# Kernel optimization log

Measured on AMD Instinct MI355X. Metric: run time of the kernel, lower is better.

Reference implementation:

```python
import jax, jax.numpy as jnp
import numpy as np

HEAD = 8
AGENT = 64  # agent_q_num = agent_kv_num = 8**2
DIM = 512


def _heads(t, head=HEAD):
    b, n, c = t.shape
    return t.reshape(b, n, head, c // head).transpose(0, 2, 1, 3)  # (b,h,n,d)


def _attn(q, k, v, pe, scale):
    # post-softmax additive bias (the non-standard part that breaks SDPA fusion)
    s = jax.nn.softmax(jnp.einsum('bhnd,bhmd->bhnm', q, k) * scale, axis=-1) + pe
    o = jnp.einsum('bhnm,bhmd->bhnd', s, v)
    b, h, n, d = o.shape
    return o.transpose(0, 2, 1, 3).reshape(b, n, h * d)


def _mlp(x, w1, b1, w2, b2):
    return jax.nn.silu(x @ w1 + b1) @ w2 + b2


def setup_inputs() -> dict:
    key = jax.random.key(0)
    ks = jax.random.split(key, 32)
    d = DIM
    inp = {
        'x': jax.random.normal(ks[0], (8, 64, 64, d), jnp.float32),
        'learnable_q': jax.random.normal(ks[1], (1, AGENT, d), jnp.float32) * 0.02,
        'learnable_kv': jax.random.normal(ks[2], (1, AGENT, d), jnp.float32) * 0.02,
        'pe1': jax.random.normal(ks[3], (1, HEAD, 1, AGENT), jnp.float32) * 0.02,
        'pe2': jax.random.normal(ks[4], (1, HEAD, AGENT, 1), jnp.float32) * 0.02,
        'w_q': jax.random.normal(ks[5], (d, d), jnp.float32) * (d ** -0.5),
        'b_q': jax.random.normal(ks[6], (d,), jnp.float32) * 0.02,
        'w_kvx': jax.random.normal(ks[7], (d, 2 * d), jnp.float32) * (d ** -0.5),
        'b_kvx': jax.random.normal(ks[8], (2 * d,), jnp.float32) * 0.02,
        'w_kvy': jax.random.normal(ks[9], (d, 2 * d), jnp.float32) * (d ** -0.5),
        'b_kvy': jax.random.normal(ks[10], (2 * d,), jnp.float32) * 0.02,
        'w_q2': jax.random.normal(ks[11], (d, d), jnp.float32) * (d ** -0.5),
        'b_q2': jax.random.normal(ks[12], (d,), jnp.float32) * 0.02,
        'f1w1': jax.random.normal(ks[13], (d, d), jnp.float32) * (d ** -0.5),
        'f1b1': jax.random.normal(ks[14], (d,), jnp.float32) * 0.02,
        'f1w2': jax.random.normal(ks[15], (d, d), jnp.float32) * (d ** -0.5),
        'f1b2': jax.random.normal(ks[16], (d,), jnp.float32) * 0.02,
        'f2w1': jax.random.normal(ks[17], (d, d), jnp.float32) * (d ** -0.5),
        'f2b1': jax.random.normal(ks[18], (d,), jnp.float32) * 0.02,
        'f2w2': jax.random.normal(ks[19], (d, d), jnp.float32) * (d ** -0.5),
        'f2b2': jax.random.normal(ks[20], (d,), jnp.float32) * 0.02,
    }
    return inp


def reference(x, learnable_q, learnable_kv, pe1, pe2, w_q, b_q, w_kvx, b_kvx,
              w_kvy, b_kvy, w_q2, b_q2, f1w1, f1b1, f1w2, f1b2,
              f2w1, f2b1, f2w2, f2b2):
    b, h, w, c = x.shape
    d = c // HEAD
    scale = d ** -0.5
    xf = x.reshape(b, h * w, c)

    # stage 1: image tokens attend to learnable proxy kv tokens
    q = _heads(xf @ w_q2 + b_q2)                                   # (b,H,hw,d)
    kv = jnp.broadcast_to(learnable_kv, (b, AGENT, c)) @ w_kvy + b_kvy
    k, v = jnp.split(kv, 2, axis=-1)
    out = _attn(q, _heads(k), _heads(v), pe1, scale)               # (b,hw,c)
    out = _mlp(out, f1w1, f1b1, f1w2, f1b2) + xf
    mskip = out

    # stage 2: learnable proxy queries attend to image tokens
    q2 = _heads(jnp.broadcast_to(learnable_q, (b, AGENT, c)) @ w_q + b_q)
    kv = out @ w_kvx + b_kvx
    k, v = jnp.split(kv, 2, axis=-1)
    fin = _attn(q2, _heads(k), _heads(v), pe2, scale)              # (b,AGENT,c)
    fin = _mlp(fin, f2w1, f2b1, f2w2, f2b2)

    # nearest-neighbor upsample 8x8 agent grid back to (h,w)
    s = int(AGENT ** 0.5)
    fin = fin.reshape(b, s, s, c)
    fin = jnp.repeat(jnp.repeat(fin, h // s, axis=1), w // s, axis=2)
    return fin + mskip.reshape(b, h, w, c) + x
```

## Files before the change

### kernel.cpp

```cpp
#include <hip/hip_runtime.h>
#include <stdint.h>

typedef unsigned short ub16;
typedef __attribute__((ext_vector_type(8))) short short8;
typedef __attribute__((ext_vector_type(4))) float f32x4;
typedef __attribute__((ext_vector_type(4))) unsigned short us4v;

__device__ __forceinline__ float bf2f(ub16 u) {
  union { unsigned int i; float f; } v; v.i = ((unsigned int)u) << 16; return v.f;
}
__device__ __forceinline__ ub16 f2bf(float f) {
  union { float f; unsigned int i; } v; v.f = f;
  return (ub16)((v.i + 0x7FFFu + ((v.i >> 16) & 1u)) >> 16);
}
__device__ __forceinline__ f32x4 zero4() { f32x4 v = {0.f, 0.f, 0.f, 0.f}; return v; }
__device__ __forceinline__ f32x4 mfma16(short8 a, short8 b, f32x4 c) {
  return __builtin_amdgcn_mfma_f32_16x16x32_bf16(a, b, c, 0, 0, 0);
}
__device__ __forceinline__ float rmax16(float x) {
  x = fmaxf(x, __shfl_xor(x, 1)); x = fmaxf(x, __shfl_xor(x, 2));
  x = fmaxf(x, __shfl_xor(x, 4)); x = fmaxf(x, __shfl_xor(x, 8)); return x;
}
__device__ __forceinline__ float rsum16(float x) {
  x += __shfl_xor(x, 1); x += __shfl_xor(x, 2);
  x += __shfl_xor(x, 4); x += __shfl_xor(x, 8); return x;
}

__device__ __forceinline__ void gload16(const ub16* g, ub16* l) {
  __builtin_amdgcn_global_load_lds(
      (const __attribute__((address_space(1))) void*)g,
      (__attribute__((address_space(3))) void*)l, 16, 0, 0);
}

__device__ __forceinline__ void stage_tile(const ub16* __restrict__ src, ub16* ldsbase,
                                           int wid, int lane) {
  const int rr = lane >> 3;
  const int slog = (lane & 7) ^ rr;
#pragma unroll
  for (int c = 0; c < 4; ++c) {
    int chunk = wid * 4 + c;
    int row = chunk * 8 + rr;
    gload16(src + (size_t)row * 512 + slog * 8,
            (ub16*)((char*)ldsbase + chunk * 1024));
  }
}

__device__ __forceinline__ void gemm_compute(const ub16* Ab, const ub16* Bb, int wm, int wn,
                                             int l15, int lg, f32x4 acc[4][4]) {
#pragma unroll
  for (int kf = 0; kf < 2; ++kf) {
    short8 af[4], bfr[4];
#pragma unroll
    for (int mf = 0; mf < 4; ++mf) {
      int row = wm * 64 + mf * 16 + l15;
      af[mf] = *(const short8*)((const char*)Ab + row * 128 +
                                ((kf * 64 + lg * 16) ^ ((row & 7) << 4)));
    }
#pragma unroll
    for (int nf = 0; nf < 4; ++nf) {
      int row = wn * 64 + nf * 16 + l15;
      bfr[nf] = *(const short8*)((const char*)Bb + row * 128 +
                                 ((kf * 64 + lg * 16) ^ ((row & 7) << 4)));
    }
#pragma unroll
    for (int mf = 0; mf < 4; ++mf)
#pragma unroll
      for (int nf = 0; nf < 4; ++nf)
        acc[mf][nf] = mfma16(af[mf], bfr[nf], acc[mf][nf]);
  }
}

__device__ __forceinline__ void gemm_k512(const ub16* Ap, const ub16* Bp, ub16* lds,
                                          int wid, int lane, int wm, int wn, int l15, int lg,
                                          f32x4 acc[4][4]) {
  ub16* A0 = lds;
  ub16* B0 = lds + 8192;
#pragma unroll
  for (int kb = 0; kb < 8; ++kb) {
    stage_tile(Ap + kb * 64, A0, wid, lane);
    stage_tile(Bp + kb * 64, B0, wid, lane);
    asm volatile("s_waitcnt vmcnt(0)" ::: "memory");
    __syncthreads();
    gemm_compute(A0, B0, wm, wn, l15, lg, acc);
    __syncthreads();
  }
}

__device__ __forceinline__ void xcd_remap(int nx, int& m0, int& n0) {
  int bid = blockIdx.x, nwg = gridDim.x;
  int cpx = nwg >> 3;
  int wgid = (bid & 7) * cpx + (bid >> 3);
  n0 = (wgid % nx) * 128;
  m0 = (wgid / nx) * 128;
}

__global__ void k_cvt(const float* __restrict__ x, ub16* __restrict__ xb) {
  int i = blockIdx.x * 256 + threadIdx.x;
  f32x4 v = *(const f32x4*)&x[(size_t)i * 4];
  us4v o;
#pragma unroll
  for (int e = 0; e < 4; ++e) o[e] = f2bf(v[e]);
  *(us4v*)&xb[(size_t)i * 4] = o;
}

__global__ void k_prep_wt(const float* s0, const float* s1, const float* s2,
                          const float* s3, const float* s4,
                          ub16* d0, ub16* d1, ub16* d2, ub16* d3, ub16* d4) {
  const float* src; ub16* dst; int N;
  switch (blockIdx.z) {
    case 0: src = s0; dst = d0; N = 512; break;
    case 1: src = s1; dst = d1; N = 512; break;
    case 2: src = s2; dst = d2; N = 512; break;
    case 3: src = s3; dst = d3; N = 512; break;
    default: src = s4; dst = d4; N = 1024; break;
  }
  int n0 = blockIdx.x * 64, k0 = blockIdx.y * 64;
  if (n0 >= N) return;
  __shared__ float tile[64][65];
#pragma unroll
  for (int i = 0; i < 16; ++i) {
    int idx = i * 256 + threadIdx.x, r = idx >> 6, c = idx & 63;
    tile[r][c] = src[(size_t)(k0 + r) * N + n0 + c];
  }
  __syncthreads();
#pragma unroll
  for (int i = 0; i < 16; ++i) {
    int idx = i * 256 + threadIdx.x, r = idx >> 6, c = idx & 63;
    dst[(size_t)(n0 + r) * 512 + k0 + c] = f2bf(tile[c][r]);
  }
}

__global__ void k_prep_small(const float* __restrict__ lkv, const float* __restrict__ w_kvy,
                             const float* __restrict__ b_kvy, const float* __restrict__ lq,
                             const float* __restrict__ w_q, const float* __restrict__ b_q,
                             const float* __restrict__ pe1,
                             ub16* __restrict__ k1, ub16* __restrict__ v1T,
                             float* __restrict__ bias1, ub16* __restrict__ q2p) {
  int j = blockIdx.x, t = threadIdx.x;
  __shared__ float wcol[512];
  __shared__ float red[64];
  const float* W; const float* src; float bias; int NC, jj;
  if (j < 1024) { W = w_kvy; NC = 1024; src = lkv; jj = j;        bias = b_kvy[j]; }
  else          { W = w_q;   NC = 512;  src = lq;  jj = j - 1024; bias = b_q[jj]; }
#pragma unroll
  for (int e = 0; e < 8; ++e) wcol[t * 8 + e] = W[(size_t)(t * 8 + e) * NC + jj];
  __syncthreads();
  float acc = bias;
  for (int k = 0; k < 512; ++k) acc += src[(size_t)t * 512 + k] * wcol[k];
  if (j < 512) {
    int h = j >> 6, d = j & 63;
    k1[(size_t)(h * 64 + t) * 64 + d] = f2bf(acc * 0.125f);
  } else if (j < 1024) {
    int h = (j - 512) >> 6, d = (j - 512) & 63;
    v1T[(size_t)(h * 64 + d) * 64 + t] = f2bf(acc);
    red[t] = pe1[h * 64 + t] * acc;
    __syncthreads();
    for (int s = 32; s > 0; s >>= 1) { if (t < s) red[t] += red[t + s]; __syncthreads(); }
    if (t == 0) bias1[h * 64 + d] = red[0];
  } else {
    int h = jj >> 6, d = jj & 63;
    q2p[(size_t)(h * 64 + t) * 64 + d] = f2bf(acc * 0.125f);
  }
}

__global__ __launch_bounds__(256) void k_prep_wqk(
    const float* __restrict__ w_q2, const float* __restrict__ b_q2,
    const ub16* __restrict__ k1, ub16* __restrict__ WqkT,
    float* __restrict__ biass) {
  int ha = blockIdx.x, h = ha >> 6, t = threadIdx.x;
  __shared__ float kr[64];
  if (t < 64) kr[t] = bf2f(k1[(size_t)ha * 64 + t]);
  __syncthreads();
#pragma unroll
  for (int i = 0; i < 2; ++i) {
    int kin = t + i * 256;
    const float* wrow = &w_q2[(size_t)kin * 512 + h * 64];
    float acc = 0.f;
#pragma unroll
    for (int d4 = 0; d4 < 16; ++d4) {
      f32x4 wv = *(const f32x4*)&wrow[d4 * 4];
      acc += wv[0] * kr[d4 * 4] + wv[1] * kr[d4 * 4 + 1] +
             wv[2] * kr[d4 * 4 + 2] + wv[3] * kr[d4 * 4 + 3];
    }
    WqkT[(size_t)ha * 512 + kin] = f2bf(acc);
  }
  if (t == 0) {
    float acc = 0.f;
    for (int d = 0; d < 64; ++d) acc += b_q2[h * 64 + d] * kr[d];
    biass[ha] = acc;
  }
}

__global__ __launch_bounds__(256) void k_s1a(
    const ub16* __restrict__ xb, const ub16* __restrict__ WqkT,
    const float* __restrict__ biass, const ub16* __restrict__ v1T,
    const float* __restrict__ bias1, ub16* __restrict__ o1) {
  __shared__ ub16 lds[16384];
  const int tid = threadIdx.x, lane = tid & 63, wid = tid >> 6;
  const int wm = wid >> 1, wn = wid & 1;
  const int l15 = lane & 15, lg = lane >> 4;
  int m0, n0;
  xcd_remap(4, m0, n0);

  f32x4 acc[4][4];
#pragma unroll
  for (int a = 0; a < 4; ++a)
#pragma unroll
    for (int b = 0; b < 4; ++b) acc[a][b] = zero4();

  gemm_k512(xb + (size_t)m0 * 512, WqkT + (size_t)n0 * 512, lds,
            wid, lane, wm, wn, l15, lg, acc);

  __syncthreads();
  const int h = (n0 >> 6) + wn;
  char* Pl = (char*)lds + wid * 8192;
  float bsv[4];
#pragma unroll
  for (int nf = 0; nf < 4; ++nf) bsv[nf] = biass[h * 64 + nf * 16 + l15];
  float dinv[4][4];
#pragma unroll
  for (int mf = 0; mf < 4; ++mf) {
#pragma unroll
    for (int r = 0; r < 4; ++r) {
      float s0 = acc[mf][0][r] + bsv[0], s1 = acc[mf][1][r] + bsv[1];
      float s2 = acc[mf][2][r] + bsv[2], s3 = acc[mf][3][r] + bsv[3];
      float mx = rmax16(fmaxf(fmaxf(s0, s1), fmaxf(s2, s3)));
      float p0 = __expf(s0 - mx), p1 = __expf(s1 - mx);
      float p2 = __expf(s2 - mx), p3 = __expf(s3 - mx);
      float sm = rsum16(p0 + p1 + p2 + p3);
      dinv[mf][r] = 1.0f / sm;
      int tr = mf * 16 + lg * 4 + r;
      char* rb = Pl + tr * 128;
      int sw = (tr & 7) << 4;
      *(ub16*)(rb + (((0 * 16 + l15) * 2) ^ sw)) = f2bf(p0);
      *(ub16*)(rb + (((1 * 16 + l15) * 2) ^ sw)) = f2bf(p1);
      *(ub16*)(rb + (((2 * 16 + l15) * 2) ^ sw)) = f2bf(p2);
      *(ub16*)(rb + (((3 * 16 + l15) * 2) ^ sw)) = f2bf(p3);
    }
  }
  short8 pa[4][2], vb[4][2];
#pragma unroll
  for (int mf = 0; mf < 4; ++mf) {
    int row = mf * 16 + l15;
#pragma unroll
    for (int kf = 0; kf < 2; ++kf)
      pa[mf][kf] = *(const short8*)(Pl + row * 128 + ((kf * 64 + lg * 16) ^ ((row & 7) << 4)));
  }
#pragma unroll
  for (int nf = 0; nf < 4; ++nf)
#pragma unroll
    for (int kf = 0; kf < 2; ++kf)
      vb[nf][kf] = *(const short8*)&v1T[(size_t)(h * 64 + nf * 16 + l15) * 64 + kf * 32 + lg * 8];
  f32x4 oacc[4][4];
#pragma unroll
  for (int a = 0; a < 4; ++a)
#pragma unroll
    for (int b = 0; b < 4; ++b) oacc[a][b] = zero4();
#pragma unroll
  for (int kf = 0; kf < 2; ++kf)
#pragma unroll
    for (int mf = 0; mf < 4; ++mf)
#pragma unroll
      for (int nf = 0; nf < 4; ++nf)
        oacc[mf][nf] = mfma16(pa[mf][kf], vb[nf][kf], oacc[mf][nf]);
  float b1v[4];
#pragma unroll
  for (int nf = 0; nf < 4; ++nf) b1v[nf] = bias1[h * 64 + nf * 16 + l15];
#pragma unroll
  for (int mf = 0; mf < 4; ++mf)
#pragma unroll
    for (int nf = 0; nf < 4; ++nf)
#pragma unroll
      for (int r = 0; r < 4; ++r) {
        float val = oacc[mf][nf][r] * dinv[mf][r] + b1v[nf];
        o1[(size_t)(m0 + wm * 64 + mf * 16 + lg * 4 + r) * 512 + h * 64 + nf * 16 + l15] = f2bf(val);
      }
}

__global__ __launch_bounds__(256) void k_mlp1a(
    const ub16* __restrict__ o1, const ub16* __restrict__ W1T,
    const float* __restrict__ b1, ub16* __restrict__ h1) {
  __shared__ ub16 lds[16384];
  const int tid = threadIdx.x, lane = tid & 63, wid = tid >> 6;
  const int wm = wid >> 1, wn = wid & 1;
  const int l15 = lane & 15, lg = lane >> 4;
  int m0, n0;
  xcd_remap(4, m0, n0);
  f32x4 acc[4][4];
#pragma unroll
  for (int a = 0; a < 4; ++a)
#pragma unroll
    for (int b = 0; b < 4; ++b) acc[a][b] = zero4();
  gemm_k512(o1 + (size_t)m0 * 512, W1T + (size_t)n0 * 512, lds,
            wid, lane, wm, wn, l15, lg, acc);
#pragma unroll
  for (int nf = 0; nf < 4; ++nf) {
    int n = n0 + wn * 64 + nf * 16 + l15;
    float bb = b1[n];
#pragma unroll
    for (int mf = 0; mf < 4; ++mf)
#pragma unroll
      for (int r = 0; r < 4; ++r) {
        float v = acc[mf][nf][r] + bb;
        v = v / (1.0f + __expf(-v));
        int m = m0 + wm * 64 + mf * 16 + lg * 4 + r;
        h1[(size_t)m * 512 + n] = f2bf(v);
      }
  }
}

__global__ __launch_bounds__(256) void k_mlp1b(
    const ub16* __restrict__ h1, const ub16* __restrict__ W2T,
    const float* __restrict__ b2, ub16* __restrict__ xb_mskip) {
  __shared__ ub16 lds[16384];
  const int tid = threadIdx.x, lane = tid & 63, wid = tid >> 6;
  const int wm = wid >> 1, wn = wid & 1;
  const int l15 = lane & 15, lg = lane >> 4;
  int m0, n0;
  xcd_remap(4, m0, n0);
  f32x4 acc[4][4];
#pragma unroll
  for (int a = 0; a < 4; ++a)
#pragma unroll
    for (int b = 0; b < 4; ++b) acc[a][b] = zero4();
  gemm_k512(h1 + (size_t)m0 * 512, W2T + (size_t)n0 * 512, lds,
            wid, lane, wm, wn, l15, lg, acc);
#pragma unroll
  for (int nf = 0; nf < 4; ++nf) {
    int n = n0 + wn * 64 + nf * 16 + l15;
    float bb = b2[n];
#pragma unroll
    for (int mf = 0; mf < 4; ++mf)
#pragma unroll
      for (int r = 0; r < 4; ++r) {
        int m = m0 + wm * 64 + mf * 16 + lg * 4 + r;
        size_t idx = (size_t)m * 512 + n;
        float val = acc[mf][nf][r] + bb + bf2f(xb_mskip[idx]);
        xb_mskip[idx] = f2bf(val);
      }
  }
}

__global__ __launch_bounds__(256) void k_mlp2b(
    const ub16* __restrict__ h2, const ub16* __restrict__ W2T,
    const float* __restrict__ b2, float* __restrict__ fin) {
  __shared__ ub16 lds[16384];
  const int tid = threadIdx.x, lane = tid & 63, wid = tid >> 6;
  const int wm = wid >> 1, wn = wid & 1;
  const int l15 = lane & 15, lg = lane >> 4;
  int m0, n0;
  xcd_remap(4, m0, n0);
  f32x4 acc[4][4];
#pragma unroll
  for (int a = 0; a < 4; ++a)
#pragma unroll
    for (int b = 0; b < 4; ++b) acc[a][b] = zero4();
  gemm_k512(h2 + (size_t)m0 * 512, W2T + (size_t)n0 * 512, lds,
            wid, lane, wm, wn, l15, lg, acc);
#pragma unroll
  for (int nf = 0; nf < 4; ++nf) {
    int n = n0 + wn * 64 + nf * 16 + l15;
    float bb = b2[n];
#pragma unroll
    for (int mf = 0; mf < 4; ++mf)
#pragma unroll
      for (int r = 0; r < 4; ++r) {
        int m = m0 + wm * 64 + mf * 16 + lg * 4 + r;
        fin[(size_t)m * 512 + n] = acc[mf][nf][r] + bb;
      }
  }
}

__global__ __launch_bounds__(256) void k_g4(
    const ub16* __restrict__ mskip_bf, const ub16* __restrict__ WT,
    const float* __restrict__ bias, ub16* __restrict__ Kb, ub16* __restrict__ VTb) {
  __shared__ ub16 lds[16384];
  const int tid = threadIdx.x, lane = tid & 63, wid = tid >> 6;
  const int wm = wid >> 1, wn = wid & 1;
  const int l15 = lane & 15, lg = lane >> 4;
  int m0, n0;
  xcd_remap(8, m0, n0);
  f32x4 acc[4][4];
#pragma unroll
  for (int a = 0; a < 4; ++a)
#pragma unroll
    for (int b = 0; b < 4; ++b) acc[a][b] = zero4();
  gemm_k512(mskip_bf + (size_t)m0 * 512, WT + (size_t)n0 * 512, lds,
            wid, lane, wm, wn, l15, lg, acc);
  const int ncb = n0 + wn * 64;
  if (n0 < 512) {
    const int hh = ncb >> 6;
#pragma unroll
    for (int mf = 0; mf < 4; ++mf)
#pragma unroll
      for (int r = 0; r < 4; ++r) {
        int m = m0 + wm * 64 + mf * 16 + lg * 4 + r;
        int b = m >> 12, t = m & 4095;
#pragma unroll
        for (int nf = 0; nf < 4; ++nf) {
          int d = nf * 16 + l15;
          Kb[((size_t)(b * 8 + hh) * 4096 + t) * 64 + d] = f2bf(acc[mf][nf][r] + bias[ncb + d]);
        }
      }
  } else {
    const int hv = (ncb >> 6) - 8;
#pragma unroll
    for (int mf = 0; mf < 4; ++mf) {
      int m4 = m0 + wm * 64 + mf * 16 + lg * 4;
      int b = m4 >> 12, t = m4 & 4095;
#pragma unroll
      for (int nf = 0; nf < 4; ++nf) {
        int d = nf * 16 + l15;
        float bb = bias[ncb + d];
        us4v pk;
#pragma unroll
        for (int r = 0; r < 4; ++r) pk[r] = f2bf(acc[mf][nf][r] + bb);
        *(us4v*)&VTb[((size_t)(b * 8 + hv) * 64 + d) * 4096 + t] = pk;
      }
    }
  }
}

__global__ __launch_bounds__(256) void k_attn2(
    const ub16* __restrict__ q2p, const ub16* __restrict__ Kb, const ub16* __restrict__ VTb,
    float* __restrict__ m_part, float* __restrict__ l_part,
    float* __restrict__ cs_part, float* __restrict__ o_part) {
  const int tid = threadIdx.x, lane = tid & 63, wid = tid >> 6;
  const int l15 = lane & 15, lg = lane >> 4;
  const int b = blockIdx.z, h = blockIdx.y;
  const int split = blockIdx.x * 4 + wid;
  __shared__ ub16 plds[4 * 64 * 40];
  ub16* pl = plds + wid * 64 * 40;
  short8 qa[4][2];
#pragma unroll
  for (int mf = 0; mf < 4; ++mf)
#pragma unroll
    for (int kf = 0; kf < 2; ++kf)
      qa[mf][kf] = *(const short8*)&q2p[(size_t)(h * 64 + mf * 16 + l15) * 64 + kf * 32 + lg * 8];
  float mr[4][4], lr[4][4], cs[4] = {0.f, 0.f, 0.f, 0.f};
  f32x4 oa[4][4];
#pragma unroll
  for (int a = 0; a < 4; ++a)
#pragma unroll
    for (int r = 0; r < 4; ++r) { mr[a][r] = -1e30f; lr[a][r] = 0.f; }
#pragma unroll
  for (int a = 0; a < 4; ++a)
#pragma unroll
    for (int n = 0; n < 4; ++n) oa[a][n] = zero4();
  const size_t kbase = (size_t)(b * 8 + h) * 4096 * 64;
  const size_t vbase = (size_t)(b * 8 + h) * 64 * 4096;
  for (int c = 0; c < 8; ++c) {
    int tb = split * 256 + c * 32;
    short8 kbf[2][2];
#pragma unroll
    for (int nf = 0; nf < 2; ++nf)
#pragma unroll
      for (int kf = 0; kf < 2; ++kf)
        kbf[nf][kf] = *(const short8*)&Kb[kbase + (size_t)(tb + nf * 16 + l15) * 64 + kf * 32 + lg * 8];
    f32x4 sc[4][2];
#pragma unroll
    for (int a = 0; a < 4; ++a)
#pragma unroll
      for (int n = 0; n < 2; ++n) sc[a][n] = zero4();
#pragma unroll
    for (int kf = 0; kf < 2; ++kf)
#pragma unroll
      for (int mf = 0; mf < 4; ++mf)
#pragma unroll
        for (int nf = 0; nf < 2; ++nf)
          sc[mf][nf] = mfma16(qa[mf][kf], kbf[nf][kf], sc[mf][nf]);
    float al[4][4];
#pragma unroll
    for (int mf = 0; mf < 4; ++mf)
#pragma unroll
      for (int r = 0; r < 4; ++r) {
        float cm = rmax16(fmaxf(sc[mf][0][r], sc[mf][1][r]));
        float nm = fmaxf(mr[mf][r], cm);
        float a_ = __expf(mr[mf][r] - nm);
        float p0 = __expf(sc[mf][0][r] - nm), p1 = __expf(sc[mf][1][r] - nm);
        float rs = rsum16(p0 + p1);
        lr[mf][r] = lr[mf][r] * a_ + rs;
        mr[mf][r] = nm;
        al[mf][r] = a_;
        int ar = mf * 16 + lg * 4 + r;
        char* rb = (char*)pl + ar * 80;
        *(ub16*)(rb + (0 * 16 + l15) * 2) = f2bf(p0);
        *(ub16*)(rb + (1 * 16 + l15) * 2) = f2bf(p1);
      }
#pragma unroll
    for (int mf = 0; mf < 4; ++mf)
#pragma unroll
      for (int nf = 0; nf < 4; ++nf)
#pragma unroll
        for (int r = 0; r < 4; ++r) oa[mf][nf][r] *= al[mf][r];
    short8 pa[4], vb[4];
#pragma unroll
    for (int mf = 0; mf < 4; ++mf)
      pa[mf] = *(const short8*)((char*)pl + (mf * 16 + l15) * 80 + lg * 16);
#pragma unroll
    for (int nf = 0; nf < 4; ++nf) {
      vb[nf] = *(const short8*)&VTb[vbase + (size_t)(nf * 16 + l15) * 4096 + tb + lg * 8];
#pragma unroll
      for (int e = 0; e < 8; ++e) cs[nf] += bf2f((ub16)vb[nf][e]);
    }
#pragma unroll
    for (int mf = 0; mf < 4; ++mf)
#pragma unroll
      for (int nf = 0; nf < 4; ++nf)
        oa[mf][nf] = mfma16(pa[mf], vb[nf], oa[mf][nf]);
  }
#pragma unroll
  for (int nf = 0; nf < 4; ++nf) {
    cs[nf] += __shfl_xor(cs[nf], 16);
    cs[nf] += __shfl_xor(cs[nf], 32);
  }
  const int pidx = (b * 8 + h) * 16 + split;
  if (lg == 0) {
#pragma unroll
    for (int nf = 0; nf < 4; ++nf) cs_part[(size_t)pidx * 64 + nf * 16 + l15] = cs[nf];
  }
  if (l15 == 0) {
#pragma unroll
    for (int mf = 0; mf < 4; ++mf)
#pragma unroll
      for (int r = 0; r < 4; ++r) {
        int a = mf * 16 + lg * 4 + r;
        m_part[(size_t)pidx * 64 + a] = mr[mf][r];
        l_part[(size_t)pidx * 64 + a] = lr[mf][r];
      }
  }
#pragma unroll
  for (int mf = 0; mf < 4; ++mf)
#pragma unroll
    for (int nf = 0; nf < 4; ++nf)
#pragma unroll
      for (int r = 0; r < 4; ++r) {
        int a = mf * 16 + lg * 4 + r, d = nf * 16 + l15;
        o_part[(size_t)pidx * 4096 + a * 64 + d] = oa[mf][nf][r];
      }
}

__global__ __launch_bounds__(256) void k_combine(
    const float* __restrict__ m_part, const float* __restrict__ l_part,
    const float* __restrict__ cs_part, const float* __restrict__ o_part,
    const float* __restrict__ pe2, ub16* __restrict__ fin0) {
  int bh = blockIdx.x, b = bh >> 3, h = bh & 7;
  int t = threadIdx.x;
  __shared__ float wsp[16][64];
  __shared__ float linv[64];
  __shared__ float cst[64];
  int base = bh * 16;
  if (t < 64) {
    int a = t;
    float M = -1e30f;
    for (int s = 0; s < 16; ++s) M = fmaxf(M, m_part[(size_t)(base + s) * 64 + a]);
    float L = 0.f;
    for (int s = 0; s < 16; ++s) {
      float w = __expf(m_part[(size_t)(base + s) * 64 + a] - M);
      wsp[s][a] = w;
      L += l_part[(size_t)(base + s) * 64 + a] * w;
    }
    linv[a] = 1.0f / L;
  } else if (t < 128) {
    int d = t - 64;
    float c = 0.f;
    for (int s = 0; s < 16; ++s) c += cs_part[(size_t)(base + s) * 64 + d];
    cst[d] = c;
  }
  __syncthreads();
#pragma unroll
  for (int e0 = 0; e0 < 4096; e0 += 256) {
    int e = e0 + t, a = e >> 6, d = e & 63;
    float acc = 0.f;
#pragma unroll
    for (int s = 0; s < 16; ++s) acc += o_part[(size_t)(base + s) * 4096 + e] * wsp[s][a];
    float val = acc * linv[a] + pe2[h * 64 + a] * cst[d];
    fin0[(size_t)(b * 64 + a) * 512 + h * 64 + d] = f2bf(val);
  }
}

__global__ void k_final(const float* __restrict__ x, const float* __restrict__ fin,
                        const ub16* __restrict__ mskip_bf, float* __restrict__ out) {
  int i = blockIdx.x * 256 + threadIdx.x;
  int e = i * 4;
  int c = e & 511, j = (e >> 9) & 63, ii = (e >> 15) & 63, b = e >> 21;
  f32x4 xv = *(const f32x4*)&x[(size_t)e];
  us4v mv = *(const us4v*)&mskip_bf[(size_t)e];
  f32x4 fv = *(const f32x4*)&fin[(size_t)((b * 64 + (ii >> 3) * 8 + (j >> 3)) << 9) + c];
  f32x4 r;
#pragma unroll
  for (int q = 0; q < 4; ++q) r[q] = xv[q] + fv[q] + bf2f(mv[q]);
  *(f32x4*)&out[(size_t)e] = r;
}

extern "C" void kernel_launch(void* const* d_in, const int* in_sizes, int n_in,
                              void* d_out, int out_size, void* d_ws, size_t ws_size,
                              hipStream_t stream) {
  const float* x     = (const float*)d_in[0];
  const float* lq    = (const float*)d_in[1];
  const float* lkv   = (const float*)d_in[2];
  const float* pe1   = (const float*)d_in[3];
  const float* pe2   = (const float*)d_in[4];
  const float* w_q   = (const float*)d_in[5];
  const float* b_q   = (const float*)d_in[6];
  const float* w_kvx = (const float*)d_in[7];
  const float* b_kvx = (const float*)d_in[8];
  const float* w_kvy = (const float*)d_in[9];
  const float* b_kvy = (const float*)d_in[10];
  const float* w_q2  = (const float*)d_in[11];
  const float* b_q2  = (const float*)d_in[12];
  const float* f1w1  = (const float*)d_in[13];
  const float* f1b1  = (const float*)d_in[14];
  const float* f1w2  = (const float*)d_in[15];
  const float* f1b2  = (const float*)d_in[16];
  const float* f2w1  = (const float*)d_in[17];
  const float* f2b1  = (const float*)d_in[18];
  const float* f2w2  = (const float*)d_in[19];
  const float* f2b2  = (const float*)d_in[20];
  float* out = (float*)d_out;

  char* ws = (char*)d_ws;
  size_t off = 0;
  auto alloc = [&](size_t bytes) {
    char* p = ws + off;
    off += (bytes + 255) & ~(size_t)255;
    return p;
  };
  ub16* xb    = (ub16*)alloc((size_t)32768 * 512 * 2);
  ub16* o1    = (ub16*)alloc((size_t)32768 * 512 * 2);
  ub16* VTb   = (ub16*)alloc((size_t)64 * 64 * 4096 * 2);
  ub16* WqkT  = (ub16*)alloc((size_t)512 * 512 * 2);
  ub16* w1T   = (ub16*)alloc((size_t)512 * 512 * 2);
  ub16* w2T   = (ub16*)alloc((size_t)512 * 512 * 2);
  ub16* g1T   = (ub16*)alloc((size_t)512 * 512 * 2);
  ub16* g2T   = (ub16*)alloc((size_t)512 * 512 * 2);
  ub16* kvxT  = (ub16*)alloc((size_t)1024 * 512 * 2);
  ub16* k1    = (ub16*)alloc((size_t)8 * 64 * 64 * 2);
  ub16* v1T   = (ub16*)alloc((size_t)8 * 64 * 64 * 2);
  ub16* q2p   = (ub16*)alloc((size_t)8 * 64 * 64 * 2);
  float* bias1 = (float*)alloc(512 * 4);
  float* biass = (float*)alloc(512 * 4);
  float* m_part = (float*)alloc((size_t)1024 * 64 * 4);
  float* l_part = (float*)alloc((size_t)1024 * 64 * 4);
  float* cs_part = (float*)alloc((size_t)1024 * 64 * 4);
  float* o_part = (float*)alloc((size_t)1024 * 4096 * 4);
  ub16* fin0 = (ub16*)alloc((size_t)512 * 512 * 2);
  float* fin = (float*)alloc((size_t)512 * 512 * 4);
  ub16* h2 = (ub16*)alloc((size_t)512 * 512 * 2);
  ub16* Kbuf = o1;
  ub16* h1buf = VTb;
  ub16* mskip_bf = xb;
  (void)in_sizes; (void)n_in; (void)out_size; (void)ws_size;

  const int n4 = (8 * 64 * 64 * 512) / 4;

  k_cvt<<<n4 / 256, 256, 0, stream>>>(x, xb);
  k_prep_wt<<<dim3(16, 8, 5), 256, 0, stream>>>(f1w1, f1w2, f2w1, f2w2, w_kvx,
                                                w1T, w2T, g1T, g2T, kvxT);
  k_prep_small<<<1536, 64, 0, stream>>>(lkv, w_kvy, b_kvy, lq, w_q, b_q, pe1,
                                        k1, v1T, bias1, q2p);
  k_prep_wqk<<<512, 256, 0, stream>>>(w_q2, b_q2, k1, WqkT, biass);
  k_s1a<<<1024, 256, 0, stream>>>(xb, WqkT, biass, v1T, bias1, o1);
  k_mlp1a<<<1024, 256, 0, stream>>>(o1, w1T, f1b1, h1buf);
  k_mlp1b<<<1024, 256, 0, stream>>>(h1buf, w2T, f1b2, mskip_bf);
  k_g4<<<2048, 256, 0, stream>>>(mskip_bf, kvxT, b_kvx, Kbuf, VTb);
  k_attn2<<<dim3(4, 8, 8), 256, 0, stream>>>(q2p, Kbuf, VTb, m_part, l_part, cs_part, o_part);
  k_combine<<<64, 256, 0, stream>>>(m_part, l_part, cs_part, o_part, pe2, fin0);
  k_mlp1a<<<16, 256, 0, stream>>>(fin0, g1T, f2b1, h2);
  k_mlp2b<<<16, 256, 0, stream>>>(h2, g2T, f2b2, fin);
  k_final<<<n4 / 256, 256, 0, stream>>>(x, fin, mskip_bf, out);
}
```

Before: 332.2 us.

## Use 256x128 tiles with 8 waves and swapped MFMA operands for vectorized epilogues

The MLP and KV projection GEMMs move from 128x128 tiles with 4 waves to 256x128 tiles with 8 waves, so each staged B tile serves twice as many rows and B-side global traffic drops. MFMA operands are swapped so each lane holds four consecutive columns, letting bias loads and output stores use 4-wide vector accesses instead of scalar strided stores. The cost is larger LDS use per block, fewer blocks in flight, and the tiny stage-2 MLP launches now use only 8 blocks.

Result: slower. 341.7 us (+2.8%).

```diff
diff --git a/kernel.cpp b/kernel.cpp
--- a/kernel.cpp
+++ b/kernel.cpp
@@ -39,6 +39,20 @@
 #pragma unroll
   for (int c = 0; c < 4; ++c) {
     int chunk = wid * 4 + c;
+    int row = chunk * 8 + rr;
+    gload16(src + (size_t)row * 512 + slog * 8,
+            (ub16*)((char*)ldsbase + chunk * 1024));
+  }
+}
+
+template<int CNT>
+__device__ __forceinline__ void stage_tile512(const ub16* __restrict__ src, ub16* ldsbase,
+                                              int wid, int lane) {
+  const int rr = lane >> 3;
+  const int slog = (lane & 7) ^ rr;
+#pragma unroll
+  for (int c = 0; c < CNT; ++c) {
+    int chunk = c * 8 + wid;
     int row = chunk * 8 + rr;
     gload16(src + (size_t)row * 512 + slog * 8,
             (ub16*)((char*)ldsbase + chunk * 1024));
@@ -86,12 +100,63 @@
   }
 }
 
+template<bool SWAP>
+__device__ __forceinline__ void gemm_compute_w8(const ub16* Ab, const ub16* Bb, int wm, int wn,
+                                                int l15, int lg, f32x4 acc[4][4]) {
+#pragma unroll
+  for (int kf = 0; kf < 2; ++kf) {
+    short8 af[4], bfr[4];
+#pragma unroll
+    for (int mf = 0; mf < 4; ++mf) {
+      int row = wm * 64 + mf * 16 + l15;
+      af[mf] = *(const short8*)((const char*)Ab + row * 128 +
+                                ((kf * 64 + lg * 16) ^ ((row & 7) << 4)));
+    }
+#pragma unroll
+    for (int nf = 0; nf < 4; ++nf) {
+      int row = wn * 64 + nf * 16 + l15;
+      bfr[nf] = *(const short8*)((const char*)Bb + row * 128 +
+                                 ((kf * 64 + lg * 16) ^ ((row & 7) << 4)));
+    }
+#pragma unroll
+    for (int mf = 0; mf < 4; ++mf)
+#pragma unroll
+      for (int nf = 0; nf < 4; ++nf)
+        acc[mf][nf] = SWAP ? mfma16(bfr[nf], af[mf], acc[mf][nf])
+                           : mfma16(af[mf], bfr[nf], acc[mf][nf]);
+  }
+}
+
+template<bool SWAP>
+__device__ __forceinline__ void gemm_k512_w8(const ub16* Ap, const ub16* Bp, ub16* lds,
+                                             int wid, int lane, int wm, int wn, int l15, int lg,
+                                             f32x4 acc[4][4]) {
+  ub16* A0 = lds;
+  ub16* B0 = lds + 16384;
+#pragma unroll
+  for (int kb = 0; kb < 8; ++kb) {
+    stage_tile512<4>(Ap + kb * 64, A0, wid, lane);
+    stage_tile512<2>(Bp + kb * 64, B0, wid, lane);
+    asm volatile("s_waitcnt vmcnt(0)" ::: "memory");
+    __syncthreads();
+    gemm_compute_w8<SWAP>(A0, B0, wm, wn, l15, lg, acc);
+    __syncthreads();
+  }
+}
+
 __device__ __forceinline__ void xcd_remap(int nx, int& m0, int& n0) {
   int bid = blockIdx.x, nwg = gridDim.x;
   int cpx = nwg >> 3;
   int wgid = (bid & 7) * cpx + (bid >> 3);
   n0 = (wgid % nx) * 128;
   m0 = (wgid / nx) * 128;
+}
+__device__ __forceinline__ void xcd_remap256(int nx, int& m0, int& n0) {
+  int bid = blockIdx.x, nwg = gridDim.x;
+  int cpx = nwg >> 3;
+  int wgid = (bid & 7) * cpx + (bid >> 3);
+  n0 = (wgid % nx) * 128;
+  m0 = (wgid / nx) * 256;
 }
 
 __global__ void k_cvt(const float* __restrict__ x, ub16* __restrict__ xb) {
@@ -277,132 +342,142 @@
       }
 }
 
-__global__ __launch_bounds__(256) void k_mlp1a(
-    const ub16* __restrict__ o1, const ub16* __restrict__ W1T,
+__global__ __launch_bounds__(512) void k_mlp1a(
+    const ub16* __restrict__ in, const ub16* __restrict__ W1T,
     const float* __restrict__ b1, ub16* __restrict__ h1) {
-  __shared__ ub16 lds[16384];
+  __shared__ ub16 lds[24576];
   const int tid = threadIdx.x, lane = tid & 63, wid = tid >> 6;
   const int wm = wid >> 1, wn = wid & 1;
   const int l15 = lane & 15, lg = lane >> 4;
   int m0, n0;
-  xcd_remap(4, m0, n0);
+  xcd_remap256(4, m0, n0);
   f32x4 acc[4][4];
 #pragma unroll
   for (int a = 0; a < 4; ++a)
 #pragma unroll
     for (int b = 0; b < 4; ++b) acc[a][b] = zero4();
-  gemm_k512(o1 + (size_t)m0 * 512, W1T + (size_t)n0 * 512, lds,
-            wid, lane, wm, wn, l15, lg, acc);
-#pragma unroll
-  for (int nf = 0; nf < 4; ++nf) {
-    int n = n0 + wn * 64 + nf * 16 + l15;
-    float bb = b1[n];
-#pragma unroll
-    for (int mf = 0; mf < 4; ++mf)
+  gemm_k512_w8<true>(in + (size_t)m0 * 512, W1T + (size_t)n0 * 512, lds,
+                     wid, lane, wm, wn, l15, lg, acc);
+#pragma unroll
+  for (int mf = 0; mf < 4; ++mf) {
+    int m = m0 + wm * 64 + mf * 16 + l15;
+#pragma unroll
+    for (int nf = 0; nf < 4; ++nf) {
+      int nb = n0 + wn * 64 + nf * 16 + lg * 4;
+      f32x4 bb = *(const f32x4*)&b1[nb];
+      us4v pk;
 #pragma unroll
       for (int r = 0; r < 4; ++r) {
-        float v = acc[mf][nf][r] + bb;
+        float v = acc[mf][nf][r] + bb[r];
         v = v / (1.0f + __expf(-v));
-        int m = m0 + wm * 64 + mf * 16 + lg * 4 + r;
-        h1[(size_t)m * 512 + n] = f2bf(v);
+        pk[r] = f2bf(v);
       }
-  }
-}
-
-__global__ __launch_bounds__(256) void k_mlp1b(
+      *(us4v*)&h1[(size_t)m * 512 + nb] = pk;
+    }
+  }
+}
+
+__global__ __launch_bounds__(512) void k_mlp1b(
     const ub16* __restrict__ h1, const ub16* __restrict__ W2T,
     const float* __restrict__ b2, ub16* __restrict__ xb_mskip) {
-  __shared__ ub16 lds[16384];
+  __shared__ ub16 lds[24576];
   const int tid = threadIdx.x, lane = tid & 63, wid = tid >> 6;
   const int wm = wid >> 1, wn = wid & 1;
   const int l15 = lane & 15, lg = lane >> 4;
   int m0, n0;
-  xcd_remap(4, m0, n0);
+  xcd_remap256(4, m0, n0);
   f32x4 acc[4][4];
 #pragma unroll
   for (int a = 0; a < 4; ++a)
 #pragma unroll
     for (int b = 0; b < 4; ++b) acc[a][b] = zero4();
-  gemm_k512(h1 + (size_t)m0 * 512, W2T + (size_t)n0 * 512, lds,
-            wid, lane, wm, wn, l15, lg, acc);
-#pragma unroll
-  for (int nf = 0; nf < 4; ++nf) {
-    int n = n0 + wn * 64 + nf * 16 + l15;
-    float bb = b2[n];
-#pragma unroll
-    for (int mf = 0; mf < 4; ++mf)
-#pragma unroll
-      for (int r = 0; r < 4; ++r) {
-        int m = m0 + wm * 64 + mf * 16 + lg * 4 + r;
-        size_t idx = (size_t)m * 512 + n;
-        float val = acc[mf][nf][r] + bb + bf2f(xb_mskip[idx]);
-        xb_mskip[idx] = f2bf(val);
-      }
-  }
-}
-
-__global__ __launch_bounds__(256) void k_mlp2b(
+  gemm_k512_w8<true>(h1 + (size_t)m0 * 512, W2T + (size_t)n0 * 512, lds,
+                     wid, lane, wm, wn, l15, lg, acc);
+#pragma unroll
+  for (int mf = 0; mf < 4; ++mf) {
+    int m = m0 + wm * 64 + mf * 16 + l15;
+#pragma unroll
+    for (int nf = 0; nf < 4; ++nf) {
+      int nb = n0 + wn * 64 + nf * 16 + lg * 4;
+      f32x4 bb = *(const f32x4*)&b2[nb];
+      size_t idx = (size_t)m * 512 + nb;
+      us4v mv = *(const us4v*)&xb_mskip[idx];
+      us4v pk;
+#pragma unroll
+      for (int r = 0; r < 4; ++r)
+        pk[r] = f2bf(acc[mf][nf][r] + bb[r] + bf2f(mv[r]));
+      *(us4v*)&xb_mskip[idx] = pk;
+    }
+  }
+}
+
+__global__ __launch_bounds__(512) void k_mlp2b(
     const ub16* __restrict__ h2, const ub16* __restrict__ W2T,
     const float* __restrict__ b2, float* __restrict__ fin) {
-  __shared__ ub16 lds[16384];
+  __shared__ ub16 lds[24576];
   const int tid = threadIdx.x, lane = tid & 63, wid = tid >> 6;
   const int wm = wid >> 1, wn = wid & 1;
   const int l15 = lane & 15, lg = lane >> 4;
   int m0, n0;
-  xcd_remap(4, m0, n0);
+  xcd_remap256(4, m0, n0);
   f32x4 acc[4][4];
 #pragma unroll
   for (int a = 0; a < 4; ++a)
 #pragma unroll
     for (int b = 0; b < 4; ++b) acc[a][b] = zero4();
-  gemm_k512(h2 + (size_t)m0 * 512, W2T + (size_t)n0 * 512, lds,
-            wid, lane, wm, wn, l15, lg, acc);
-#pragma unroll
-  for (int nf = 0; nf < 4; ++nf) {
-    int n = n0 + wn * 64 + nf * 16 + l15;
-    float bb = b2[n];
-#pragma unroll
-    for (int mf = 0; mf < 4; ++mf)
-#pragma unroll
-      for (int r = 0; r < 4; ++r) {
-        int m = m0 + wm * 64 + mf * 16 + lg * 4 + r;
-        fin[(size_t)m * 512 + n] = acc[mf][nf][r] + bb;
-      }
-  }
-}
-
-__global__ __launch_bounds__(256) void k_g4(
+  gemm_k512_w8<true>(h2 + (size_t)m0 * 512, W2T + (size_t)n0 * 512, lds,
+                     wid, lane, wm, wn, l15, lg, acc);
+#pragma unroll
+  for (int mf = 0; mf < 4; ++mf) {
+    int m = m0 + wm * 64 + mf * 16 + l15;
+#pragma unroll
+    for (int nf = 0; nf < 4; ++nf) {
+      int nb = n0 + wn * 64 + nf * 16 + lg * 4;
+      f32x4 bb = *(const f32x4*)&b2[nb];
+      f32x4 ov;
+#pragma unroll
+      for (int r = 0; r < 4; ++r) ov[r] = acc[mf][nf][r] + bb[r];
+      *(f32x4*)&fin[(size_t)m * 512 + nb] = ov;
+    }
+  }
+}
+
+__global__ __launch_bounds__(512) void k_g4(
     const ub16* __restrict__ mskip_bf, const ub16* __restrict__ WT,
     const float* __restrict__ bias, ub16* __restrict__ Kb, ub16* __restrict__ VTb) {
-  __shared__ ub16 lds[16384];
+  __shared__ ub16 lds[24576];
   const int tid = threadIdx.x, lane = tid & 63, wid = tid >> 6;
   const int wm = wid >> 1, wn = wid & 1;
   const int l15 = lane & 15, lg = lane >> 4;
   int m0, n0;
-  xcd_remap(8, m0, n0);
+  xcd_remap256(8, m0, n0);
   f32x4 acc[4][4];
 #pragma unroll
   for (int a = 0; a < 4; ++a)
 #pragma unroll
     for (int b = 0; b < 4; ++b) acc[a][b] = zero4();
-  gemm_k512(mskip_bf + (size_t)m0 * 512, WT + (size_t)n0 * 512, lds,
-            wid, lane, wm, wn, l15, lg, acc);
   const int ncb = n0 + wn * 64;
   if (n0 < 512) {
+    gemm_k512_w8<true>(mskip_bf + (size_t)m0 * 512, WT + (size_t)n0 * 512, lds,
+                       wid, lane, wm, wn, l15, lg, acc);
     const int hh = ncb >> 6;
 #pragma unroll
-    for (int mf = 0; mf < 4; ++mf)
-#pragma unroll
-      for (int r = 0; r < 4; ++r) {
-        int m = m0 + wm * 64 + mf * 16 + lg * 4 + r;
-        int b = m >> 12, t = m & 4095;
-#pragma unroll
-        for (int nf = 0; nf < 4; ++nf) {
-          int d = nf * 16 + l15;
-          Kb[((size_t)(b * 8 + hh) * 4096 + t) * 64 + d] = f2bf(acc[mf][nf][r] + bias[ncb + d]);
-        }
+    for (int mf = 0; mf < 4; ++mf) {
+      int m = m0 + wm * 64 + mf * 16 + l15;
+      int b = m >> 12, t = m & 4095;
+#pragma unroll
+      for (int nf = 0; nf < 4; ++nf) {
+        int d0 = nf * 16 + lg * 4;
+        f32x4 bb = *(const f32x4*)&bias[ncb + d0];
+        us4v pk;
+#pragma unroll
+        for (int r = 0; r < 4; ++r) pk[r] = f2bf(acc[mf][nf][r] + bb[r]);
+        *(us4v*)&Kb[((size_t)(b * 8 + hh) * 4096 + t) * 64 + d0] = pk;
       }
+    }
   } else {
+    gemm_k512_w8<false>(mskip_bf + (size_t)m0 * 512, WT + (size_t)n0 * 512, lds,
+                        wid, lane, wm, wn, l15, lg, acc);
     const int hv = (ncb >> 6) - 8;
 #pragma unroll
     for (int mf = 0; mf < 4; ++mf) {
@@ -661,12 +736,12 @@
                                         k1, v1T, bias1, q2p);
   k_prep_wqk<<<512, 256, 0, stream>>>(w_q2, b_q2, k1, WqkT, biass);
   k_s1a<<<1024, 256, 0, stream>>>(xb, WqkT, biass, v1T, bias1, o1);
-  k_mlp1a<<<1024, 256, 0, stream>>>(o1, w1T, f1b1, h1buf);
-  k_mlp1b<<<1024, 256, 0, stream>>>(h1buf, w2T, f1b2, mskip_bf);
-  k_g4<<<2048, 256, 0, stream>>>(mskip_bf, kvxT, b_kvx, Kbuf, VTb);
+  k_mlp1a<<<512, 512, 0, stream>>>(o1, w1T, f1b1, h1buf);
+  k_mlp1b<<<512, 512, 0, stream>>>(h1buf, w2T, f1b2, mskip_bf);
+  k_g4<<<1024, 512, 0, stream>>>(mskip_bf, kvxT, b_kvx, Kbuf, VTb);
   k_attn2<<<dim3(4, 8, 8), 256, 0, stream>>>(q2p, Kbuf, VTb, m_part, l_part, cs_part, o_part);
   k_combine<<<64, 256, 0, stream>>>(m_part, l_part, cs_part, o_part, pe2, fin0);
-  k_mlp1a<<<16, 256, 0, stream>>>(fin0, g1T, f2b1, h2);
-  k_mlp2b<<<16, 256, 0, stream>>>(h2, g2T, f2b2, fin);
+  k_mlp1a<<<8, 512, 0, stream>>>(fin0, g1T, f2b1, h2);
+  k_mlp2b<<<8, 512, 0, stream>>>(h2, g2T, f2b2, fin);
   k_final<<<n4 / 256, 256, 0, stream>>>(x, fin, mskip_bf, out);
 }
```

## Fuse fp32-to-bf16 conversion of x into stage-1 GEMM and vectorize epilogues

Applied to the files above, without the earlier changes.

Removes the standalone k_cvt pass by having k_s1a load fp32 x directly and convert to bf16 while staging into LDS. The mlp1b residual now reads fp32 x instead of the bf16 copy. GEMM epilogues swap MFMA operand order so each lane holds four consecutive columns, which allows vectorized bias loads and 8/16-byte stores. This trades the async global_load_lds path for synchronous register loads of the A tile in k_s1a, which may reduce load/compute overlap.

Result: no change. 327.3 us (-1.5%).

```diff
diff --git a/kernel.cpp b/kernel.cpp
--- a/kernel.cpp
+++ b/kernel.cpp
@@ -45,6 +45,25 @@
   }
 }
 
+__device__ __forceinline__ void stage_a_f32(const float* __restrict__ src, ub16* ldsbase,
+                                            int wid, int lane) {
+  const int rr = lane >> 3;
+  const int slot = lane & 7;
+#pragma unroll
+  for (int c = 0; c < 4; ++c) {
+    int chunk = wid * 4 + c;
+    int row = chunk * 8 + rr;
+    const float* g = src + (size_t)row * 512 + slot * 8;
+    f32x4 v0 = *(const f32x4*)g;
+    f32x4 v1 = *(const f32x4*)(g + 4);
+    short8 sv;
+#pragma unroll
+    for (int e = 0; e < 4; ++e) { sv[e] = (short)f2bf(v0[e]); sv[4 + e] = (short)f2bf(v1[e]); }
+    *(short8*)((char*)ldsbase + row * 128 + ((slot * 16) ^ ((row & 7) << 4))) = sv;
+  }
+}
+
+template<bool SWAP>
 __device__ __forceinline__ void gemm_compute(const ub16* Ab, const ub16* Bb, int wm, int wn,
                                              int l15, int lg, f32x4 acc[4][4]) {
 #pragma unroll
@@ -66,10 +85,12 @@
     for (int mf = 0; mf < 4; ++mf)
 #pragma unroll
       for (int nf = 0; nf < 4; ++nf)
-        acc[mf][nf] = mfma16(af[mf], bfr[nf], acc[mf][nf]);
-  }
-}
-
+        acc[mf][nf] = SWAP ? mfma16(bfr[nf], af[mf], acc[mf][nf])
+                           : mfma16(af[mf], bfr[nf], acc[mf][nf]);
+  }
+}
+
+template<bool SWAP>
 __device__ __forceinline__ void gemm_k512(const ub16* Ap, const ub16* Bp, ub16* lds,
                                           int wid, int lane, int wm, int wn, int l15, int lg,
                                           f32x4 acc[4][4]) {
@@ -81,7 +102,23 @@
     stage_tile(Bp + kb * 64, B0, wid, lane);
     asm volatile("s_waitcnt vmcnt(0)" ::: "memory");
     __syncthreads();
-    gemm_compute(A0, B0, wm, wn, l15, lg, acc);
+    gemm_compute<SWAP>(A0, B0, wm, wn, l15, lg, acc);
+    __syncthreads();
+  }
+}
+
+__device__ __forceinline__ void gemm_k512_af32(const float* Ap, const ub16* Bp, ub16* lds,
+                                               int wid, int lane, int wm, int wn, int l15, int lg,
+                                               f32x4 acc[4][4]) {
+  ub16* A0 = lds;
+  ub16* B0 = lds + 8192;
+#pragma unroll
+  for (int kb = 0; kb < 8; ++kb) {
+    stage_tile(Bp + kb * 64, B0, wid, lane);
+    stage_a_f32(Ap + kb * 64, A0, wid, lane);
+    asm volatile("s_waitcnt vmcnt(0)" ::: "memory");
+    __syncthreads();
+    gemm_compute<false>(A0, B0, wm, wn, l15, lg, acc);
     __syncthreads();
   }
 }
@@ -92,15 +129,6 @@
   int wgid = (bid & 7) * cpx + (bid >> 3);
   n0 = (wgid % nx) * 128;
   m0 = (wgid / nx) * 128;
-}
-
-__global__ void k_cvt(const float* __restrict__ x, ub16* __restrict__ xb) {
-  int i = blockIdx.x * 256 + threadIdx.x;
-  f32x4 v = *(const f32x4*)&x[(size_t)i * 4];
-  us4v o;
-#pragma unroll
-  for (int e = 0; e < 4; ++e) o[e] = f2bf(v[e]);
-  *(us4v*)&xb[(size_t)i * 4] = o;
 }
 
 __global__ void k_prep_wt(const float* s0, const float* s1, const float* s2,
@@ -192,7 +220,7 @@
 }
 
 __global__ __launch_bounds__(256) void k_s1a(
-    const ub16* __restrict__ xb, const ub16* __restrict__ WqkT,
+    const float* __restrict__ x, const ub16* __restrict__ WqkT,
     const float* __restrict__ biass, const ub16* __restrict__ v1T,
     const float* __restrict__ bias1, ub16* __restrict__ o1) {
   __shared__ ub16 lds[16384];
@@ -208,8 +236,8 @@
 #pragma unroll
     for (int b = 0; b < 4; ++b) acc[a][b] = zero4();
 
-  gemm_k512(xb + (size_t)m0 * 512, WqkT + (size_t)n0 * 512, lds,
-            wid, lane, wm, wn, l15, lg, acc);
+  gemm_k512_af32(x + (size_t)m0 * 512, WqkT + (size_t)n0 * 512, lds,
+                 wid, lane, wm, wn, l15, lg, acc);
 
   __syncthreads();
   const int h = (n0 >> 6) + wn;
@@ -278,7 +306,7 @@
 }
 
 __global__ __launch_bounds__(256) void k_mlp1a(
-    const ub16* __restrict__ o1, const ub16* __restrict__ W1T,
+    const ub16* __restrict__ in, const ub16* __restrict__ W1T,
     const float* __restrict__ b1, ub16* __restrict__ h1) {
   __shared__ ub16 lds[16384];
   const int tid = threadIdx.x, lane = tid & 63, wid = tid >> 6;
@@ -291,27 +319,31 @@
   for (int a = 0; a < 4; ++a)
 #pragma unroll
     for (int b = 0; b < 4; ++b) acc[a][b] = zero4();
-  gemm_k512(o1 + (size_t)m0 * 512, W1T + (size_t)n0 * 512, lds,
-            wid, lane, wm, wn, l15, lg, acc);
-#pragma unroll
-  for (int nf = 0; nf < 4; ++nf) {
-    int n = n0 + wn * 64 + nf * 16 + l15;
-    float bb = b1[n];
-#pragma unroll
-    for (int mf = 0; mf < 4; ++mf)
+  gemm_k512<true>(in + (size_t)m0 * 512, W1T + (size_t)n0 * 512, lds,
+                  wid, lane, wm, wn, l15, lg, acc);
+#pragma unroll
+  for (int mf = 0; mf < 4; ++mf) {
+    int m = m0 + wm * 64 + mf * 16 + l15;
+#pragma unroll
+    for (int nf = 0; nf < 4; ++nf) {
+      int nb = n0 + wn * 64 + nf * 16 + lg * 4;
+      f32x4 bb = *(const f32x4*)&b1[nb];
+      us4v pk;
 #pragma unroll
       for (int r = 0; r < 4; ++r) {
-        float v = acc[mf][nf][r] + bb;
+        float v = acc[mf][nf][r] + bb[r];
         v = v / (1.0f + __expf(-v));
-        int m = m0 + wm * 64 + mf * 16 + lg * 4 + r;
-        h1[(size_t)m * 512 + n] = f2bf(v);
+        pk[r] = f2bf(v);
       }
+      *(us4v*)&h1[(size_t)m * 512 + nb] = pk;
+    }
   }
 }
 
 __global__ __launch_bounds__(256) void k_mlp1b(
     const ub16* __restrict__ h1, const ub16* __restrict__ W2T,
-    const float* __restrict__ b2, ub16* __restrict__ xb_mskip) {
+    const float* __restrict__ b2, const float* __restrict__ x,
+    ub16* __restrict__ mskip) {
   __shared__ ub16 lds[16384];
   const int tid = threadIdx.x, lane = tid & 63, wid = tid >> 6;
   const int wm = wid >> 1, wn = wid & 1;
@@ -323,21 +355,22 @@
   for (int a = 0; a < 4; ++a)
 #pragma unroll
     for (int b = 0; b < 4; ++b) acc[a][b] = zero4();
-  gemm_k512(h1 + (size_t)m0 * 512, W2T + (size_t)n0 * 512, lds,
-            wid, lane, wm, wn, l15, lg, acc);
-#pragma unroll
-  for (int nf = 0; nf < 4; ++nf) {
-    int n = n0 + wn * 64 + nf * 16 + l15;
-    float bb = b2[n];
-#pragma unroll
-    for (int mf = 0; mf < 4; ++mf)
-#pragma unroll
-      for (int r = 0; r < 4; ++r) {
-        int m = m0 + wm * 64 + mf * 16 + lg * 4 + r;
-        size_t idx = (size_t)m * 512 + n;
-        float val = acc[mf][nf][r] + bb + bf2f(xb_mskip[idx]);
-        xb_mskip[idx] = f2bf(val);
-      }
+  gemm_k512<true>(h1 + (size_t)m0 * 512, W2T + (size_t)n0 * 512, lds,
+                  wid, lane, wm, wn, l15, lg, acc);
+#pragma unroll
+  for (int mf = 0; mf < 4; ++mf) {
+    int m = m0 + wm * 64 + mf * 16 + l15;
+#pragma unroll
+    for (int nf = 0; nf < 4; ++nf) {
+      int nb = n0 + wn * 64 + nf * 16 + lg * 4;
+      f32x4 bb = *(const f32x4*)&b2[nb];
+      f32x4 xv = *(const f32x4*)&x[(size_t)m * 512 + nb];
+      us4v pk;
+#pragma unroll
+      for (int r = 0; r < 4; ++r)
+        pk[r] = f2bf(acc[mf][nf][r] + bb[r] + xv[r]);
+      *(us4v*)&mskip[(size_t)m * 512 + nb] = pk;
+    }
   }
 }
 
@@ -355,19 +388,20 @@
   for (int a = 0; a < 4; ++a)
 #pragma unroll
     for (int b = 0; b < 4; ++b) acc[a][b] = zero4();
-  gemm_k512(h2 + (size_t)m0 * 512, W2T + (size_t)n0 * 512, lds,
-            wid, lane, wm, wn, l15, lg, acc);
-#pragma unroll
-  for (int nf = 0; nf < 4; ++nf) {
-    int n = n0 + wn * 64 + nf * 16 + l15;
-    float bb = b2[n];
-#pragma unroll
-    for (int mf = 0; mf < 4; ++mf)
-#pragma unroll
-      for (int r = 0; r < 4; ++r) {
-        int m = m0 + wm * 64 + mf * 16 + lg * 4 + r;
-        fin[(size_t)m * 512 + n] = acc[mf][nf][r] + bb;
-      }
+  gemm_k512<true>(h2 + (size_t)m0 * 512, W2T + (size_t)n0 * 512, lds,
+                  wid, lane, wm, wn, l15, lg, acc);
+#pragma unroll
+  for (int mf = 0; mf < 4; ++mf) {
+    int m = m0 + wm * 64 + mf * 16 + l15;
+#pragma unroll
+    for (int nf = 0; nf < 4; ++nf) {
+      int nb = n0 + wn * 64 + nf * 16 + lg * 4;
+      f32x4 bb = *(const f32x4*)&b2[nb];
+      f32x4 ov;
+#pragma unroll
+      for (int r = 0; r < 4; ++r) ov[r] = acc[mf][nf][r] + bb[r];
+      *(f32x4*)&fin[(size_t)m * 512 + nb] = ov;
+    }
   }
 }
 
@@ -385,24 +419,28 @@
   for (int a = 0; a < 4; ++a)
 #pragma unroll
     for (int b = 0; b < 4; ++b) acc[a][b] = zero4();
-  gemm_k512(mskip_bf + (size_t)m0 * 512, WT + (size_t)n0 * 512, lds,
-            wid, lane, wm, wn, l15, lg, acc);
   const int ncb = n0 + wn * 64;
   if (n0 < 512) {
+    gemm_k512<true>(mskip_bf + (size_t)m0 * 512, WT + (size_t)n0 * 512, lds,
+                    wid, lane, wm, wn, l15, lg, acc);
     const int hh = ncb >> 6;
 #pragma unroll
-    for (int mf = 0; mf < 4; ++mf)
-#pragma unroll
-      for (int r = 0; r < 4; ++r) {
-        int m = m0 + wm * 64 + mf * 16 + lg * 4 + r;
-        int b = m >> 12, t = m & 4095;
-#pragma unroll
-        for (int nf = 0; nf < 4; ++nf) {
-          int d = nf * 16 + l15;
-          Kb[((size_t)(b * 8 + hh) * 4096 + t) * 64 + d] = f2bf(acc[mf][nf][r] + bias[ncb + d]);
-        }
+    for (int mf = 0; mf < 4; ++mf) {
+      int m = m0 + wm * 64 + mf * 16 + l15;
+      int b = m >> 12, t = m & 4095;
+#pragma unroll
+      for (int nf = 0; nf < 4; ++nf) {
+        int d0 = nf * 16 + lg * 4;
+        f32x4 bb = *(const f32x4*)&bias[ncb + d0];
+        us4v pk;
+#pragma unroll
+        for (int r = 0; r < 4; ++r) pk[r] = f2bf(acc[mf][nf][r] + bb[r]);
+        *(us4v*)&Kb[((size_t)(b * 8 + hh) * 4096 + t) * 64 + d0] = pk;
       }
+    }
   } else {
+    gemm_k512<false>(mskip_bf + (size_t)m0 * 512, WT + (size_t)n0 * 512, lds,
+                     wid, lane, wm, wn, l15, lg, acc);
     const int hv = (ncb >> 6) - 8;
 #pragma unroll
     for (int mf = 0; mf < 4; ++mf) {
@@ -626,7 +664,7 @@
     off += (bytes + 255) & ~(size_t)255;
     return p;
   };
-  ub16* xb    = (ub16*)alloc((size_t)32768 * 512 * 2);
+  ub16* mskip_bf = (ub16*)alloc((size_t)32768 * 512 * 2);
   ub16* o1    = (ub16*)alloc((size_t)32768 * 512 * 2);
   ub16* VTb   = (ub16*)alloc((size_t)64 * 64 * 4096 * 2);
   ub16* WqkT  = (ub16*)alloc((size_t)512 * 512 * 2);
@@ -649,20 +687,18 @@
   ub16* h2 = (ub16*)alloc((size_t)512 * 512 * 2);
   ub16* Kbuf = o1;
   ub16* h1buf = VTb;
-  ub16* mskip_bf = xb;
   (void)in_sizes; (void)n_in; (void)out_size; (void)ws_size;
 
   const int n4 = (8 * 64 * 64 * 512) / 4;
 
-  k_cvt<<<n4 / 256, 256, 0, stream>>>(x, xb);
   k_prep_wt<<<dim3(16, 8, 5), 256, 0, stream>>>(f1w1, f1w2, f2w1, f2w2, w_kvx,
                                                 w1T, w2T, g1T, g2T, kvxT);
   k_prep_small<<<1536, 64, 0, stream>>>(lkv, w_kvy, b_kvy, lq, w_q, b_q, pe1,
                                         k1, v1T, bias1, q2p);
   k_prep_wqk<<<512, 256, 0, stream>>>(w_q2, b_q2, k1, WqkT, biass);
-  k_s1a<<<1024, 256, 0, stream>>>(xb, WqkT, biass, v1T, bias1, o1);
+  k_s1a<<<1024, 256, 0, stream>>>(x, WqkT, biass, v1T, bias1, o1);
   k_mlp1a<<<1024, 256, 0, stream>>>(o1, w1T, f1b1, h1buf);
-  k_mlp1b<<<1024, 256, 0, stream>>>(h1buf, w2T, f1b2, mskip_bf);
+  k_mlp1b<<<1024, 256, 0, stream>>>(h1buf, w2T, f1b2, x, mskip_bf);
   k_g4<<<2048, 256, 0, stream>>>(mskip_bf, kvxT, b_kvx, Kbuf, VTb);
   k_attn2<<<dim3(4, 8, 8), 256, 0, stream>>>(q2p, Kbuf, VTb, m_part, l_part, cs_part, o_part);
   k_combine<<<64, 256, 0, stream>>>(m_part, l_part, cs_part, o_part, pe2, fin0);
```
